# Performance work log

Measured on AMD Instinct MI355X. Metric: run time of the kernel, lower is better.

The kernel has to match this reference:

```python
import jax, jax.numpy as jnp
import numpy as np

# config constants
H = 1024          # hidden_size
I = 512           # moe_intermediate_size
IS = 1024         # moe_shared_expert_intermediate_size
E = 16            # n_routed_experts
G = 4             # n_group
TOPK_G = 2        # topk_group
TOPK = 4          # num_experts_per_tok
SCALE = 2.5       # routed_scaling_factor
B, S = 2, 1024


def _relu2(x):
    r = jax.nn.relu(x)
    return r * r


def setup_inputs() -> dict:
    key = jax.random.key(0)
    ks = jax.random.split(key, 8)
    sd = 0.02
    return {
        "hidden_states": jax.random.normal(ks[0], (B, S, H), jnp.float32),
        "Wg": jax.random.normal(ks[1], (E, H), jnp.float32) * sd,          # router gate weight
        "bias_corr": jax.random.normal(ks[2], (E,), jnp.float32) * 0.01,    # e_score_correction_bias
        "W1": jax.random.normal(ks[3], (E, I, H), jnp.float32) * sd,        # experts up_proj
        "W2": jax.random.normal(ks[4], (E, H, I), jnp.float32) * sd,        # experts down_proj
        "Ws1": jax.random.normal(ks[5], (IS, H), jnp.float32) * sd,         # shared up_proj
        "Ws2": jax.random.normal(ks[6], (H, IS), jnp.float32) * sd,         # shared down_proj
    }


def _route(scores, bias_corr):
    # scores: (T,E) = sigmoid(router logits)
    T = scores.shape[0]
    s_choice = scores + bias_corr                                           # (T,E)
    gs = s_choice.reshape(T, G, E // G)
    group_scores = jnp.sum(jax.lax.top_k(gs, 2)[0], axis=-1)                # (T,G) sum of top-2 per group
    gidx = jax.lax.top_k(group_scores, TOPK_G)[1]                           # (T,topk_group)
    gmask = jnp.sum(jax.nn.one_hot(gidx, G, dtype=scores.dtype), axis=1)    # (T,G)
    smask = jnp.repeat(gmask, E // G, axis=1)                               # (T,E)
    masked = jnp.where(smask > 0, s_choice, 0.0)
    topk_idx = jax.lax.top_k(masked, TOPK)[1]                               # (T,top_k)
    topk_w = jnp.take_along_axis(scores, topk_idx, axis=1)                  # weights from raw sigmoid scores
    topk_w = topk_w / (jnp.sum(topk_w, axis=-1, keepdims=True) + 1e-20)     # norm_topk_prob
    topk_w = topk_w * SCALE
    return topk_idx, topk_w


def reference(hidden_states, Wg, bias_corr, W1, W2, Ws1, Ws2):
    b, s, h = hidden_states.shape
    flat = hidden_states.reshape(-1, h)                                     # (T,H)
    T = flat.shape[0]
    logits = flat.astype(jnp.float32) @ Wg.T                                # (T,E)
    scores = jax.nn.sigmoid(logits)
    topk_idx, topk_w = _route(scores, bias_corr)
    topk_w = topk_w.astype(hidden_states.dtype)
    # combined per-(token, expert) weight; zero where not routed (equivalent
    # to the per-expert gather/MLP/weighted index_add in the original)
    cw = jnp.zeros((T, E), flat.dtype)
    cw = cw.at[jnp.arange(T)[:, None], topk_idx].add(topk_w)                # (T,E)
    # fc1_latent_proj / fc2_latent_proj are Identity (moe_latent_size=None)
    hid = _relu2(jnp.einsum('th,eih->eti', flat, W1))                       # (E,T,I)
    y = jnp.einsum('eti,ehi->eth', hid, W2)                                 # (E,T,H)
    out = jnp.einsum('eth,te->th', y, cw)                                   # (T,H)
    shared = _relu2(flat @ Ws1.T) @ Ws2.T                                   # shared expert on residuals
    return (out + shared).reshape(b, s, h)
```

## Files before the change

### kernel.cpp

```cpp
#include <hip/hip_runtime.h>
#include <hip/hip_bf16.h>

#define T_TOK 2048
#define HDIM 1024
#define IDIM 512
#define ISDIM 1024
#define NEXP 16
#define TOPK 4
#define NSLOT (T_TOK*TOPK)
#define SCALE_F 2.5f

typedef unsigned short u16;
typedef float f32x4 __attribute__((ext_vector_type(4)));
typedef __bf16 bf16x8 __attribute__((ext_vector_type(8)));
typedef u16 u16x8 __attribute__((ext_vector_type(8)));

__device__ __forceinline__ u16 f2bf(float f) {
  unsigned u = __builtin_bit_cast(unsigned, f);
  u += 0x7fffu + ((u >> 16) & 1u);
  return (u16)(u >> 16);
}

__device__ __forceinline__ float bf2f(u16 h) {
  unsigned u = ((unsigned)h) << 16;
  return __builtin_bit_cast(float, u);
}

__device__ __forceinline__ void gload_lds16(const u16* g, u16* l) {
  __builtin_amdgcn_global_load_lds(
      (const __attribute__((address_space(1))) void*)g,
      (__attribute__((address_space(3))) void*)l, 16, 0, 0);
}

__device__ __forceinline__ f32x4 mfma16(u16x8 a, u16x8 b, f32x4 c) {
  return __builtin_amdgcn_mfma_f32_16x16x32_bf16(
      __builtin_bit_cast(bf16x8, a), __builtin_bit_cast(bf16x8, b), c, 0, 0, 0);
}

__device__ __forceinline__ void wait_vm6()   { asm volatile("s_waitcnt vmcnt(6)" ::: "memory"); }
__device__ __forceinline__ void wait_vm0()   { asm volatile("s_waitcnt vmcnt(0)" ::: "memory"); }
__device__ __forceinline__ void wait_lgkm0() { asm volatile("s_waitcnt lgkmcnt(0)" ::: "memory"); }

#define JMAX0 136
#define G0T (8*JMAX0)
#define JMAX1 240
#define G1T (8*JMAX1)
#define MAXG0 96
#define MAXG1 192

__global__ void __launch_bounds__(256) router_kernel(
    const float* __restrict__ x, const float* __restrict__ Wg,
    const float* __restrict__ bias,
    int* __restrict__ topk_idx, float* __restrict__ topk_w,
    u16* __restrict__ Xbf) {
  int t = blockIdx.x;
  int tid = threadIdx.x;
  int lane = tid & 63;
  int wave = tid >> 6;

  __shared__ __align__(16) float sx[HDIM];
  __shared__ float ssc[NEXP];

  float4 xv = reinterpret_cast<const float4*>(x + (size_t)t * HDIM)[tid];
  reinterpret_cast<float4*>(sx)[tid] = xv;
  ushort4 o;
  o.x = f2bf(xv.x); o.y = f2bf(xv.y); o.z = f2bf(xv.z); o.w = f2bf(xv.w);
  reinterpret_cast<ushort4*>(Xbf + (size_t)t * HDIM)[tid] = o;
  __syncthreads();

  float acc[4] = {0.f, 0.f, 0.f, 0.f};
  const float4* sx4 = reinterpret_cast<const float4*>(sx);
#pragma unroll
  for (int c = 0; c < 4; c++) {
    float4 xq = sx4[lane + 64 * c];
#pragma unroll
    for (int e = 0; e < 4; e++) {
      float4 wq = reinterpret_cast<const float4*>(
          Wg + (size_t)(wave * 4 + e) * HDIM)[lane + 64 * c];
      acc[e] += xq.x * wq.x + xq.y * wq.y + xq.z * wq.z + xq.w * wq.w;
    }
  }
#pragma unroll
  for (int e = 0; e < 4; e++) {
    float v = acc[e];
#pragma unroll
    for (int off = 32; off > 0; off >>= 1) v += __shfl_xor(v, off);
    if (lane == 0) ssc[wave * 4 + e] = v;
  }
  __syncthreads();

  if (tid == 0) {
    float scores[NEXP], sc[NEXP];
#pragma unroll
    for (int e = 0; e < NEXP; e++) {
      float s = 1.f / (1.f + expf(-ssc[e]));
      scores[e] = s;
      sc[e] = s + bias[e];
    }
    float gsum[4];
#pragma unroll
    for (int g = 0; g < 4; g++) {
      float a = sc[4*g], b = sc[4*g+1], c = sc[4*g+2], d = sc[4*g+3];
      float hi1 = fmaxf(a, b), lo1 = fminf(a, b);
      float hi2 = fmaxf(c, d), lo2 = fminf(c, d);
      gsum[g] = fmaxf(hi1, hi2) + fmaxf(fminf(hi1, hi2), fmaxf(lo1, lo2));
    }
    int g0 = 0; float bv = gsum[0];
#pragma unroll
    for (int g = 1; g < 4; g++) if (gsum[g] > bv) { bv = gsum[g]; g0 = g; }
    int g1 = -1; float bv2 = -1e30f;
#pragma unroll
    for (int g = 0; g < 4; g++) if (g != g0 && gsum[g] > bv2) { bv2 = gsum[g]; g1 = g; }
    float m[NEXP];
#pragma unroll
    for (int e = 0; e < NEXP; e++) {
      int g = e >> 2;
      m[e] = (g == g0 || g == g1) ? sc[e] : 0.0f;
    }
    int idx[TOPK]; float w[TOPK];
#pragma unroll
    for (int k = 0; k < TOPK; k++) {
      int bj = 0; float bmv = m[0];
#pragma unroll
      for (int j = 1; j < NEXP; j++) if (m[j] > bmv) { bmv = m[j]; bj = j; }
      idx[k] = bj; w[k] = scores[bj];
#pragma unroll
      for (int j = 0; j < NEXP; j++) m[j] = (j == bj) ? -1e30f : m[j];
    }
    float s4 = w[0] + w[1] + w[2] + w[3] + 1e-20f;
    float inv = SCALE_F / s4;
#pragma unroll
    for (int k = 0; k < TOPK; k++) {
      topk_idx[t * TOPK + k] = idx[k];
      topk_w[t * TOPK + k] = w[k] * inv;
    }
  }
}

__global__ void __launch_bounds__(256) route_build(
    const int* __restrict__ topk_idx, const float* __restrict__ topk_w,
    int* __restrict__ offsets, int* __restrict__ counts,
    int* __restrict__ perm_token, float* __restrict__ perm_w,
    int* __restrict__ slot_of,
    int* __restrict__ tiles0, int* __restrict__ tiles1) {
  __shared__ int hcnt[NEXP];
  __shared__ int hfill[NEXP];
  __shared__ int g0s[MAXG0], g0c[MAXG0], g0n[MAXG0];
  __shared__ int g1s[MAXG1], g1c[MAXG1], g1n[MAXG1];
  __shared__ int sng0, sng1;
  int tid = threadIdx.x;
  int lane = tid & 63;
  if (tid < NEXP) hcnt[tid] = 0;
  __syncthreads();

  int e_loc[NSLOT / 256];
#pragma unroll
  for (int i = 0; i < NSLOT / 256; i++) {
    int j = tid + 256 * i;
    int e = topk_idx[j];
    e_loc[i] = e;
    unsigned long long m = ~0ull;
#pragma unroll
    for (int b = 0; b < 4; b++) {
      unsigned long long bb = __ballot((e >> b) & 1);
      m &= ((e >> b) & 1) ? bb : ~bb;
    }
    int leader = __ffsll((unsigned long long)m) - 1;
    if (lane == leader) atomicAdd(&hcnt[e], __popcll(m));
  }
  __syncthreads();

  if (tid == 0) {
    int s = 0;
#pragma unroll
    for (int e = 0; e < NEXP; e++) {
      int c = hcnt[e];
      offsets[e] = s;
      counts[e] = c;
      hfill[e] = s;
      s += c;
    }
  }
  __syncthreads();

#pragma unroll
  for (int i = 0; i < NSLOT / 256; i++) {
    int j = tid + 256 * i;
    int e = e_loc[i];
    unsigned long long m = ~0ull;
#pragma unroll
    for (int b = 0; b < 4; b++) {
      unsigned long long bb = __ballot((e >> b) & 1);
      m &= ((e >> b) & 1) ? bb : ~bb;
    }
    int leader = __ffsll((unsigned long long)m) - 1;
    int rank = __popcll(m & ((1ull << lane) - 1ull));
    int base = 0;
    if (lane == leader) base = atomicAdd(&hfill[e], __popcll(m));
    base = __shfl(base, leader);
    int pos = base + rank;
    perm_token[pos] = j >> 2;
    perm_w[pos] = topk_w[j];
    slot_of[j] = pos;
  }
  __syncthreads();

  if (tid == 0) {
    int l0=0,l1=0,l2=0,l3=0,l4=0,l5=0,l6=0,l7=0;
    int ng = 0;
#define PLACE0(code0, cn)                                               \
    { int x = 0, lv = l0;                                               \
      if (l1<lv){lv=l1;x=1;} if (l2<lv){lv=l2;x=2;}                     \
      if (l3<lv){lv=l3;x=3;} if (l4<lv){lv=l4;x=4;}                     \
      if (l5<lv){lv=l5;x=5;} if (l6<lv){lv=l6;x=6;}                     \
      if (l7<lv){lv=l7;x=7;}                                            \
      g0s[ng] = x + 8*lv; g0c[ng] = (code0); g0n[ng] = (cn); ng++;      \
      if (x==0)l0+=(cn); else if (x==1)l1+=(cn); else if (x==2)l2+=(cn);\
      else if (x==3)l3+=(cn); else if (x==4)l4+=(cn);                   \
      else if (x==5)l5+=(cn); else if (x==6)l6+=(cn); else l7+=(cn); }
    for (int nb = 0; nb < 8; nb++) PLACE0((16 << 10) | nb, 32);
    for (int e = 0; e < NEXP; e++) {
      int mc = (hcnt[e] + 63) >> 6;
      for (int nb = 0; nb < 4; nb++)
        for (int base = 0; base < mc; base += 32)
          PLACE0((e << 10) | (base << 3) | nb, min(32, mc - base));
    }
    sng0 = ng;
#undef PLACE0
  }
  if (tid == 64) {
    int l0=0,l1=0,l2=0,l3=0,l4=0,l5=0,l6=0,l7=0;
    int ng = 0;
#define PLACE1(code0, cn)                                               \
    { int x = 0, lv = l0;                                               \
      if (l1<lv){lv=l1;x=1;} if (l2<lv){lv=l2;x=2;}                     \
      if (l3<lv){lv=l3;x=3;} if (l4<lv){lv=l4;x=4;}                     \
      if (l5<lv){lv=l5;x=5;} if (l6<lv){lv=l6;x=6;}                     \
      if (l7<lv){lv=l7;x=7;}                                            \
      g1s[ng] = x + 8*lv; g1c[ng] = (code0); g1n[ng] = (cn); ng++;      \
      if (x==0)l0+=(cn); else if (x==1)l1+=(cn); else if (x==2)l2+=(cn);\
      else if (x==3)l3+=(cn); else if (x==4)l4+=(cn);                   \
      else if (x==5)l5+=(cn); else if (x==6)l6+=(cn); else l7+=(cn); }
    for (int eh = 16; eh <= 17; eh++)
      for (int nb = 0; nb < 8; nb++) PLACE1((eh << 10) | nb, 32);
    for (int e = 0; e < NEXP; e++) {
      int mc = (hcnt[e] + 63) >> 6;
      for (int nb = 0; nb < 8; nb++)
        for (int base = 0; base < mc; base += 32)
          PLACE1((e << 10) | (base << 3) | nb, min(32, mc - base));
    }
    sng1 = ng;
#undef PLACE1
  }
  if (tid >= 128) {
    for (int i = tid - 128; i < G0T; i += 128) tiles0[i] = -1;
    for (int i = tid - 128; i < G1T; i += 128) tiles1[i] = -1;
  }
  __syncthreads();

  int ng0 = sng0, ng1 = sng1;
  for (int g = tid; g < ng0; g += 256) {
    int st = g0s[g], c0 = g0c[g], cn = g0n[g];
    for (int mm = 0; mm < cn; mm++) tiles0[st + 8 * mm] = c0 + (mm << 3);
  }
  for (int g = tid; g < ng1; g += 256) {
    int st = g1s[g], c0 = g1c[g], cn = g1n[g];
    for (int mm = 0; mm < cn; mm++) tiles1[st + 8 * mm] = c0 + (mm << 3);
  }
}

#define N1Q (NEXP*IDIM*HDIM/4)
#define NSQ (ISDIM*HDIM/4)
__global__ void __launch_bounds__(256) cvt_all(
    const float* __restrict__ W1, const float* __restrict__ W2,
    const float* __restrict__ Ws1, const float* __restrict__ Ws2,
    u16* __restrict__ W1b, u16* __restrict__ W2b,
    u16* __restrict__ Ws1b, u16* __restrict__ Ws2b) {
  int i = blockIdx.x * 256 + threadIdx.x;
  const float* src; u16* dst; int off;
  if (i < N1Q)               { src = W1;  dst = W1b;  off = i; }
  else if (i < 2 * N1Q)      { src = W2;  dst = W2b;  off = i - N1Q; }
  else if (i < 2 * N1Q + NSQ){ src = Ws1; dst = Ws1b; off = i - 2 * N1Q; }
  else                       { src = Ws2; dst = Ws2b; off = i - 2 * N1Q - NSQ; }
  float4 v = reinterpret_cast<const float4*>(src)[off];
  ushort4 o;
  o.x = f2bf(v.x); o.y = f2bf(v.y); o.z = f2bf(v.z); o.w = f2bf(v.w);
  reinterpret_cast<ushort4*>(dst)[off] = o;
}

#define BM 64
#define BN 128
#define BK 64

template<int PHASE>
__global__ void __launch_bounds__(256) moe_gemm(
    const int* __restrict__ tiles,
    const u16* __restrict__ Xbf, const u16* __restrict__ Hg,
    const u16* __restrict__ Hs,
    const u16* __restrict__ W1b, const u16* __restrict__ W2b,
    const u16* __restrict__ Ws1b, const u16* __restrict__ Ws2b,
    const int* __restrict__ eoffs, const int* __restrict__ ecnts,
    const int* __restrict__ rowmap, const float* __restrict__ rowscale,
    u16* __restrict__ HgOut, u16* __restrict__ HsOut,
    u16* __restrict__ Ygb, float* __restrict__ Ys)
{
  constexpr int KL = (PHASE == 0) ? HDIM : IDIM;
  constexpr int NT = KL / BK;

  int code = tiles[blockIdx.x];
  if (code < 0) return;
  int e  = code >> 10;
  int mb = (code >> 3) & 127;
  int nb = code & 7;

  bool sh = (e >= NEXP);
  int half = e - NEXP;
  int N, Mloc, rowbase, Astr, Bstr, kb;
  const u16* Abase;
  const u16* Bp;
  if (PHASE == 0) {
    Astr = HDIM; Bstr = HDIM; kb = 0;
    if (sh) { N = ISDIM; Mloc = T_TOK; rowbase = 0; Abase = Xbf; Bp = Ws1b; }
    else    { N = IDIM; Mloc = ecnts[e]; rowbase = eoffs[e]; Abase = Xbf;
              Bp = W1b + (size_t)e * IDIM * HDIM; }
  } else {
    N = HDIM;
    if (sh) { Astr = ISDIM; Bstr = ISDIM; kb = half * IDIM;
              Mloc = T_TOK; rowbase = 0; Abase = Hs; Bp = Ws2b; }
    else    { Astr = IDIM; Bstr = IDIM; kb = 0;
              Mloc = ecnts[e]; rowbase = eoffs[e]; Abase = Hg;
              Bp = W2b + (size_t)e * HDIM * IDIM; }
  }
  int m0 = mb * BM;
  if (m0 >= Mloc) return;
  int n0 = nb * BN;
  if (n0 >= N) return;

  __shared__ __align__(16) u16 sA[2][BM * BK];
  __shared__ __align__(16) u16 sB[2][BN * BK];

  int tid = threadIdx.x;
  int lane = tid & 63;
  int wave = tid >> 6;
  int wm = (wave >> 1) * 32;
  int wn = (wave & 1) * 64;
  int fm = lane & 15;
  int kq = lane >> 4;
  int fsw = fm & 7;

  int lrow8 = lane >> 3;
  int sch = ((lane & 7) ^ lrow8) * 8;

  const u16* AgP[2];
  int aoff[2];
#pragma unroll
  for (int g = 0; g < 2; g++) {
    int rt = 16 * wave + 8 * g + lrow8;
    int ar = m0 + rt;
    int arc = (ar < Mloc) ? ar : (Mloc - 1);
    size_t asrc;
    if (PHASE == 0 && !sh) asrc = (size_t)rowmap[rowbase + arc] * Astr;
    else                   asrc = (size_t)((sh ? 0 : rowbase) + arc) * Astr;
    AgP[g] = Abase + asrc + kb + sch;
    aoff[g] = (16 * wave + 8 * g) * BK;
  }
  const u16* BgP[4];
  int boff[4];
#pragma unroll
  for (int g = 0; g < 4; g++) {
    int rt = 32 * wave + 8 * g + lrow8;
    BgP[g] = Bp + (size_t)(n0 + rt) * Bstr + kb + sch;
    boff[g] = (32 * wave + 8 * g) * BK;
  }

  f32x4 acc[2][4] = {};

#pragma unroll
  for (int g = 0; g < 2; g++) gload_lds16(AgP[g], &sA[0][aoff[g]]);
#pragma unroll
  for (int g = 0; g < 4; g++) gload_lds16(BgP[g], &sB[0][boff[g]]);
#pragma unroll
  for (int g = 0; g < 2; g++) gload_lds16(AgP[g] + BK, &sA[1][aoff[g]]);
#pragma unroll
  for (int g = 0; g < 4; g++) gload_lds16(BgP[g] + BK, &sB[1][boff[g]]);

  for (int t = 0; t < NT - 1; ++t) {
    int cur = t & 1;
    wait_vm6();
    __builtin_amdgcn_s_barrier();
    u16x8 af[2][2], bf[2][4];
#pragma unroll
    for (int ks = 0; ks < 2; ks++) {
      int ch = ((ks * 4 + kq) ^ fsw) * 8;
#pragma unroll
      for (int i = 0; i < 2; i++)
        af[ks][i] = *reinterpret_cast<const u16x8*>(&sA[cur][(wm + 16 * i + fm) * BK + ch]);
#pragma unroll
      for (int j = 0; j < 4; j++)
        bf[ks][j] = *reinterpret_cast<const u16x8*>(&sB[cur][(wn + 16 * j + fm) * BK + ch]);
    }
    wait_lgkm0();
    __builtin_amdgcn_sched_barrier(0);
    __builtin_amdgcn_s_barrier();
    if (t + 2 < NT) {
#pragma unroll
      for (int g = 0; g < 2; g++) gload_lds16(AgP[g] + (t + 2) * BK, &sA[cur][aoff[g]]);
#pragma unroll
      for (int g = 0; g < 4; g++) gload_lds16(BgP[g] + (t + 2) * BK, &sB[cur][boff[g]]);
    }
#pragma unroll
    for (int ks = 0; ks < 2; ks++)
#pragma unroll
      for (int i = 0; i < 2; i++)
#pragma unroll
        for (int j = 0; j < 4; j++)
          acc[i][j] = mfma16(af[ks][i], bf[ks][j], acc[i][j]);
  }
  {
    constexpr int cur = (NT - 1) & 1;
    wait_vm0();
    __builtin_amdgcn_s_barrier();
    u16x8 af[2][2], bf[2][4];
#pragma unroll
    for (int ks = 0; ks < 2; ks++) {
      int ch = ((ks * 4 + kq) ^ fsw) * 8;
#pragma unroll
      for (int i = 0; i < 2; i++)
        af[ks][i] = *reinterpret_cast<const u16x8*>(&sA[cur][(wm + 16 * i + fm) * BK + ch]);
#pragma unroll
      for (int j = 0; j < 4; j++)
        bf[ks][j] = *reinterpret_cast<const u16x8*>(&sB[cur][(wn + 16 * j + fm) * BK + ch]);
    }
    wait_lgkm0();
    __builtin_amdgcn_sched_barrier(0);
#pragma unroll
    for (int ks = 0; ks < 2; ks++)
#pragma unroll
      for (int i = 0; i < 2; i++)
#pragma unroll
        for (int j = 0; j < 4; j++)
          acc[i][j] = mfma16(af[ks][i], bf[ks][j], acc[i][j]);
  }

#pragma unroll
  for (int i = 0; i < 2; i++) {
#pragma unroll
    for (int r = 0; r < 4; r++) {
      int gm = m0 + wm + 16 * i + kq * 4 + r;
      if (gm < Mloc) {
        float rs = 0.f;
        if (PHASE == 0 && !sh) rs = rowscale[rowbase + gm];
#pragma unroll
        for (int j = 0; j < 4; j++) {
          int gn = n0 + wn + 16 * j + fm;
          float v = acc[i][j][r];
          if (PHASE == 0) {
            float tq = fmaxf(v, 0.f);
            if (!sh) {
              tq = tq * tq * rs;
              HgOut[(size_t)(rowbase + gm) * IDIM + gn] = f2bf(tq);
            } else {
              HsOut[(size_t)gm * ISDIM + gn] = f2bf(tq * tq);
            }
          } else {
            if (!sh) Ygb[(size_t)(rowbase + gm) * HDIM + gn] = f2bf(v);
            else     Ys[(size_t)(half * T_TOK + gm) * HDIM + gn] = v;
          }
        }
      }
    }
  }
}

__global__ void __launch_bounds__(256) combine_kernel(
    const u16* __restrict__ Ygb, const float* __restrict__ Ys,
    const int* __restrict__ slot_of, float* __restrict__ out) {
  int t = blockIdx.x;
  int i = threadIdx.x;
  int4 s = *reinterpret_cast<const int4*>(&slot_of[t * 4]);
  const ushort4* Y4 = reinterpret_cast<const ushort4*>(Ygb);
  const float4* S4 = reinterpret_cast<const float4*>(Ys);
  float4* O4 = reinterpret_cast<float4*>(out);
  float4 v0 = S4[(size_t)t * 256 + i];
  float4 v1 = S4[(size_t)(T_TOK + t) * 256 + i];
  ushort4 a = Y4[(size_t)s.x * 256 + i];
  ushort4 b = Y4[(size_t)s.y * 256 + i];
  ushort4 c = Y4[(size_t)s.z * 256 + i];
  ushort4 d = Y4[(size_t)s.w * 256 + i];
  float4 v;
  v.x = v0.x + v1.x + bf2f(a.x) + bf2f(b.x) + bf2f(c.x) + bf2f(d.x);
  v.y = v0.y + v1.y + bf2f(a.y) + bf2f(b.y) + bf2f(c.y) + bf2f(d.y);
  v.z = v0.z + v1.z + bf2f(a.z) + bf2f(b.z) + bf2f(c.z) + bf2f(d.z);
  v.w = v0.w + v1.w + bf2f(a.w) + bf2f(b.w) + bf2f(c.w) + bf2f(d.w);
  O4[(size_t)t * 256 + i] = v;
}

extern "C" void kernel_launch(void* const* d_in, const int* in_sizes, int n_in,
                              void* d_out, int out_size, void* d_ws, size_t ws_size,
                              hipStream_t stream) {
  const float* x    = (const float*)d_in[0];
  const float* Wg   = (const float*)d_in[1];
  const float* bias = (const float*)d_in[2];
  const float* W1   = (const float*)d_in[3];
  const float* W2   = (const float*)d_in[4];
  const float* Ws1  = (const float*)d_in[5];
  const float* Ws2  = (const float*)d_in[6];
  float* out = (float*)d_out;

  char* p = (char*)d_ws;
  auto alloc = [&](size_t bytes) -> void* {
    void* r = (void*)p;
    p += (bytes + 255) & ~(size_t)255;
    return r;
  };
  int*   topk_idx   = (int*)  alloc((size_t)NSLOT * 4);
  float* topk_w     = (float*)alloc((size_t)NSLOT * 4);
  int*   counts     = (int*)  alloc(64);
  int*   offsets    = (int*)  alloc(64);
  int*   perm_token = (int*)  alloc((size_t)NSLOT * 4);
  float* perm_w     = (float*)alloc((size_t)NSLOT * 4);
  int*   slot_of    = (int*)  alloc((size_t)NSLOT * 4);
  int*   tiles0     = (int*)  alloc((size_t)G0T * 4);
  int*   tiles1     = (int*)  alloc((size_t)G1T * 4);
  u16*   Xbf        = (u16*)  alloc((size_t)T_TOK * HDIM * 2);
  u16*   W1b        = (u16*)  alloc((size_t)NEXP * IDIM * HDIM * 2);
  u16*   W2b        = (u16*)  alloc((size_t)NEXP * HDIM * IDIM * 2);
  u16*   Ws1b      = (u16*)  alloc((size_t)ISDIM * HDIM * 2);
  u16*   Ws2b      = (u16*)  alloc((size_t)HDIM * ISDIM * 2);
  u16*   Hg         = (u16*)  alloc((size_t)NSLOT * IDIM * 2);
  u16*   Hs         = (u16*)  alloc((size_t)T_TOK * ISDIM * 2);
  u16*   Ygb        = (u16*)  alloc((size_t)NSLOT * HDIM * 2);
  float* Ys         = (float*)alloc((size_t)2 * T_TOK * HDIM * 4);

  router_kernel<<<T_TOK, 256, 0, stream>>>(x, Wg, bias, topk_idx, topk_w, Xbf);
  route_build<<<1, 256, 0, stream>>>(topk_idx, topk_w, offsets, counts,
                                     perm_token, perm_w, slot_of,
                                     tiles0, tiles1);

  cvt_all<<<(2 * N1Q + 2 * NSQ + 255) / 256, 256, 0, stream>>>(
      W1, W2, Ws1, Ws2, W1b, W2b, Ws1b, Ws2b);

  moe_gemm<0><<<G0T, 256, 0, stream>>>(
      tiles0, Xbf, Hg, Hs, W1b, W2b, Ws1b, Ws2b, offsets, counts,
      perm_token, perm_w, Hg, Hs, nullptr, nullptr);

  moe_gemm<1><<<G1T, 256, 0, stream>>>(
      tiles1, Xbf, Hg, Hs, W1b, W2b, Ws1b, Ws2b, offsets, counts,
      perm_token, perm_w, Hg, Hs, Ygb, Ys);

  combine_kernel<<<T_TOK, 256, 0, stream>>>(Ygb, Ys, slot_of, out);
}
```

Before: 256.2 us.

## Split single-block route build into parallel histogram and scatter kernels

Replaces the single-workgroup routing build with a 32-block histogram kernel using global atomics, followed by a 33-block kernel. In that kernel 32 blocks scatter slots in parallel and the last block builds the tile schedules. Counters are zeroed by the router kernel's first block. The aim is to remove the serial latency of one block walking all 8192 slots, at the cost of an extra kernel launch and global atomics. Slot order within each expert is now nondeterministic.

```diff
diff --git a/kernel.cpp b/kernel.cpp
--- a/kernel.cpp
+++ b/kernel.cpp
@@ -52,11 +52,14 @@
     const float* __restrict__ x, const float* __restrict__ Wg,
     const float* __restrict__ bias,
     int* __restrict__ topk_idx, float* __restrict__ topk_w,
-    u16* __restrict__ Xbf) {
+    u16* __restrict__ Xbf,
+    int* __restrict__ counts, int* __restrict__ gfill) {
   int t = blockIdx.x;
   int tid = threadIdx.x;
   int lane = tid & 63;
   int wave = tid >> 6;
+
+  if (t == 0 && tid < NEXP) { counts[tid] = 0; gfill[tid] = 0; }
 
   __shared__ __align__(16) float sx[HDIM];
   __shared__ float ssc[NEXP];
@@ -137,72 +140,68 @@
   }
 }
 
-__global__ void __launch_bounds__(256) route_build(
+__global__ void __launch_bounds__(256) hist_kernel(
+    const int* __restrict__ topk_idx, int* __restrict__ counts) {
+  int j = blockIdx.x * 256 + threadIdx.x;
+  int lane = threadIdx.x & 63;
+  int e = topk_idx[j];
+  unsigned long long m = ~0ull;
+#pragma unroll
+  for (int b = 0; b < 4; b++) {
+    unsigned long long bb = __ballot((e >> b) & 1);
+    m &= ((e >> b) & 1) ? bb : ~bb;
+  }
+  int leader = __ffsll(m) - 1;
+  if (lane == leader) atomicAdd(&counts[e], __popcll(m));
+}
+
+__global__ void __launch_bounds__(256) scatter_build(
     const int* __restrict__ topk_idx, const float* __restrict__ topk_w,
-    int* __restrict__ offsets, int* __restrict__ counts,
+    const int* __restrict__ counts, int* __restrict__ offsets,
+    int* __restrict__ gfill,
     int* __restrict__ perm_token, float* __restrict__ perm_w,
     int* __restrict__ slot_of,
     int* __restrict__ tiles0, int* __restrict__ tiles1) {
+  int b = blockIdx.x;
+  int tid = threadIdx.x;
+  int lane = tid & 63;
+
+  if (b < 32) {
+    int c = (lane < NEXP) ? counts[lane] : 0;
+    int incl = c;
+#pragma unroll
+    for (int o = 1; o < 16; o <<= 1) {
+      int v = __shfl_up(incl, o);
+      if (lane >= o) incl += v;
+    }
+    int excl = incl - c;
+
+    int j = b * 256 + tid;
+    int e = topk_idx[j];
+    unsigned long long m = ~0ull;
+#pragma unroll
+    for (int bb = 0; bb < 4; bb++) {
+      unsigned long long bl = __ballot((e >> bb) & 1);
+      m &= ((e >> bb) & 1) ? bl : ~bl;
+    }
+    int leader = __ffsll(m) - 1;
+    int rank = __popcll(m & ((1ull << lane) - 1ull));
+    int base = 0;
+    if (lane == leader) base = atomicAdd(&gfill[e], __popcll(m));
+    base = __shfl(base, leader);
+    int pos = __shfl(excl, e) + base + rank;
+    perm_token[pos] = j >> 2;
+    perm_w[pos] = topk_w[j];
+    slot_of[j] = pos;
+    if (b == 0 && tid < NEXP) offsets[tid] = excl;
+    return;
+  }
+
   __shared__ int hcnt[NEXP];
-  __shared__ int hfill[NEXP];
   __shared__ int g0s[MAXG0], g0c[MAXG0], g0n[MAXG0];
   __shared__ int g1s[MAXG1], g1c[MAXG1], g1n[MAXG1];
   __shared__ int sng0, sng1;
-  int tid = threadIdx.x;
-  int lane = tid & 63;
-  if (tid < NEXP) hcnt[tid] = 0;
-  __syncthreads();
-
-  int e_loc[NSLOT / 256];
-#pragma unroll
-  for (int i = 0; i < NSLOT / 256; i++) {
-    int j = tid + 256 * i;
-    int e = topk_idx[j];
-    e_loc[i] = e;
-    unsigned long long m = ~0ull;
-#pragma unroll
-    for (int b = 0; b < 4; b++) {
-      unsigned long long bb = __ballot((e >> b) & 1);
-      m &= ((e >> b) & 1) ? bb : ~bb;
-    }
-    int leader = __ffsll((unsigned long long)m) - 1;
-    if (lane == leader) atomicAdd(&hcnt[e], __popcll(m));
-  }
-  __syncthreads();
-
-  if (tid == 0) {
-    int s = 0;
-#pragma unroll
-    for (int e = 0; e < NEXP; e++) {
-      int c = hcnt[e];
-      offsets[e] = s;
-      counts[e] = c;
-      hfill[e] = s;
-      s += c;
-    }
-  }
-  __syncthreads();
-
-#pragma unroll
-  for (int i = 0; i < NSLOT / 256; i++) {
-    int j = tid + 256 * i;
-    int e = e_loc[i];
-    unsigned long long m = ~0ull;
-#pragma unroll
-    for (int b = 0; b < 4; b++) {
-      unsigned long long bb = __ballot((e >> b) & 1);
-      m &= ((e >> b) & 1) ? bb : ~bb;
-    }
-    int leader = __ffsll((unsigned long long)m) - 1;
-    int rank = __popcll(m & ((1ull << lane) - 1ull));
-    int base = 0;
-    if (lane == leader) base = atomicAdd(&hfill[e], __popcll(m));
-    base = __shfl(base, leader);
-    int pos = base + rank;
-    perm_token[pos] = j >> 2;
-    perm_w[pos] = topk_w[j];
-    slot_of[j] = pos;
-  }
+  if (tid < NEXP) hcnt[tid] = counts[tid];
   __syncthreads();
 
   if (tid == 0) {
@@ -517,6 +516,7 @@
   float* topk_w     = (float*)alloc((size_t)NSLOT * 4);
   int*   counts     = (int*)  alloc(64);
   int*   offsets    = (int*)  alloc(64);
+  int*   gfill      = (int*)  alloc(64);
   int*   perm_token = (int*)  alloc((size_t)NSLOT * 4);
   float* perm_w     = (float*)alloc((size_t)NSLOT * 4);
   int*   slot_of    = (int*)  alloc((size_t)NSLOT * 4);
@@ -532,10 +532,12 @@
   u16*   Ygb        = (u16*)  alloc((size_t)NSLOT * HDIM * 2);
   float* Ys         = (float*)alloc((size_t)2 * T_TOK * HDIM * 4);
 
-  router_kernel<<<T_TOK, 256, 0, stream>>>(x, Wg, bias, topk_idx, topk_w, Xbf);
-  route_build<<<1, 256, 0, stream>>>(topk_idx, topk_w, offsets, counts,
-                                     perm_token, perm_w, slot_of,
-                                     tiles0, tiles1);
+  router_kernel<<<T_TOK, 256, 0, stream>>>(x, Wg, bias, topk_idx, topk_w, Xbf,
+                                           counts, gfill);
+  hist_kernel<<<32, 256, 0, stream>>>(topk_idx, counts);
+  scatter_build<<<33, 256, 0, stream>>>(topk_idx, topk_w, counts, offsets,
+                                        gfill, perm_token, perm_w, slot_of,
+                                        tiles0, tiles1);
 
   cvt_all<<<(2 * N1Q + 2 * NSQ + 255) / 256, 256, 0, stream>>>(
       W1, W2, Ws1, Ws2, W1b, W2b, Ws1b, Ws2b);
```

Measured after the change: 234.6 us. -8.4%, faster.
